# Kernel optimization log

Hardware: AMD Instinct MI355X
Metric: run time of the kernel (lower is better)

## Reference

```python
import jax, jax.numpy as jnp
import numpy as np
import math

B, S, V, E, D, H, L = 1024, 30, 100000, 300, 512, 8, 4
DK = D // H

def setup_inputs() -> dict:
    key = jax.random.key(0)
    ks = jax.random.split(key, 12)
    sc = 0.02
    return {
        "x": jax.random.randint(ks[0], (B, S), 0, V, dtype=jnp.int32),
        "mask": jax.random.randint(ks[1], (B, 1, 1, S), 0, 2, dtype=jnp.int32),
        "emb": jax.random.normal(ks[2], (V, E), dtype=jnp.float32) * sc,
        "W_in": jax.random.normal(ks[3], (D, E), dtype=jnp.float32) * sc,
        "b_in": jnp.zeros((D,), jnp.float32),
        "Wq": jax.random.normal(ks[4], (L, DK, DK), dtype=jnp.float32) * 0.05,
        "Wk": jax.random.normal(ks[5], (L, DK, DK), dtype=jnp.float32) * 0.05,
        "Wv": jax.random.normal(ks[6], (L, DK, DK), dtype=jnp.float32) * 0.05,
        "Wo": jax.random.normal(ks[7], (L, D, D), dtype=jnp.float32) * sc,
        "Wfc": jax.random.normal(ks[8], (L, D, D), dtype=jnp.float32) * sc,
        "bfc": jnp.zeros((L, D), jnp.float32),
        "g1": jnp.ones((L, D), jnp.float32),
        "beta1": jnp.zeros((L, D), jnp.float32),
        "g2": jnp.ones((L, D), jnp.float32),
        "beta2": jnp.zeros((L, D), jnp.float32),
    }

def _layernorm(x, g, b, eps=1e-5):
    mu = jnp.mean(x, axis=-1, keepdims=True)
    var = jnp.mean(jnp.square(x - mu), axis=-1, keepdims=True)
    return (x - mu) * jax.lax.rsqrt(var + eps) * g + b

def _pos_encoding():
    pos = jnp.arange(S, dtype=jnp.float32)[:, None]
    div = jnp.exp(jnp.arange(0, D, 2, dtype=jnp.float32) * (-math.log(10000.0) / D))
    ang = pos * div  # [S, D/2]
    pe = jnp.zeros((S, D), jnp.float32)
    pe = pe.at[:, 0::2].set(jnp.sin(ang)).at[:, 1::2].set(jnp.cos(ang))
    return pe

def _block(h, mask, Wq, Wk, Wv, Wo, Wfc, bfc, g1, b1, g2, b2):
    xh = h.reshape(B, S, H, DK)
    # per-head shared d_k x d_k projections (nn.Linear: y = x @ W.T)
    q = jnp.einsum('bshk,dk->bhsd', xh, Wq)
    k = jnp.einsum('bshk,dk->bhsd', xh, Wk)
    v = jnp.einsum('bshk,dk->bhsd', xh, Wv)
    scores = jnp.einsum('bhqd,bhkd->bhqk', q, k) / math.sqrt(DK)
    scores = jnp.where(mask == 0, jnp.float32(-1e9), scores)
    p = jax.nn.softmax(scores, axis=-1)
    o = jnp.einsum('bhqk,bhkd->bqhd', p, v).reshape(B, S, D)
    o = o @ Wo.T  # output projection, no bias
    n1 = _layernorm(o + h, g1, b1)
    f = n1 @ Wfc.T + bfc
    return _layernorm(f + n1, g2, b2)

def reference(x, mask, emb, W_in, b_in, Wq, Wk, Wv, Wo, Wfc, bfc, g1, beta1, g2, beta2):
    h = emb[x]                               # [B,S,E] embedding gather
    h = jnp.einsum('bse,de->bsd', h, W_in) + b_in
    h = h * math.sqrt(D) + _pos_encoding()[None]  # positional encoding (dropout=eval no-op)
    for i in range(L):
        h = _block(h, mask, Wq[i], Wk[i], Wv[i], Wo[i], Wfc[i], bfc[i],
                   g1[i], beta1[i], g2[i], beta2[i])
    return h
```

## Files before the change

### kernel.cpp

```cpp
#include <hip/hip_runtime.h>
#include <hip/hip_bf16.h>
#include <math.h>

using bf16 = __hip_bfloat16;
typedef __attribute__((ext_vector_type(8))) short short8;
typedef __attribute__((ext_vector_type(4))) float f32x4;

constexpr int nB = 1024, nS = 30, nE = 300, nD = 512, nH = 8, nL = 4, nDK = 64;
constexpr int nTOK = nB * nS;
constexpr float kSqrtD = 22.627416997969522f;
constexpr float kPEc   = -0.03597789207803244f;

__device__ inline unsigned short bfbits(float f) {
  bf16 h = __float2bfloat16(f);
  return *(unsigned short*)&h;
}
__device__ inline void gload16(const void* g, void* lds) {
  __builtin_amdgcn_global_load_lds(
      (const __attribute__((address_space(1))) unsigned int*)g,
      (__attribute__((address_space(3))) unsigned int*)lds, 16, 0, 0);
}

__global__ __launch_bounds__(256) void cvt_kernel(const float* __restrict__ s,
                                                  bf16* __restrict__ d, int n4) {
  int i = blockIdx.x * 256 + threadIdx.x;
  if (i < n4) {
    float4 v = ((const float4*)s)[i];
    ushort4 u;
    u.x = bfbits(v.x); u.y = bfbits(v.y); u.z = bfbits(v.z); u.w = bfbits(v.w);
    ((ushort4*)d)[i] = u;
  }
}

__global__ __launch_bounds__(256) void cvt_pad_win(const float* __restrict__ s,
                                                   bf16* __restrict__ d) {
  int row = blockIdx.x;
  for (int e = threadIdx.x; e < 320; e += 256)
    d[row * 320 + e] = __float2bfloat16((e < nE) ? s[row * nE + e] : 0.f);
}

__global__ __launch_bounds__(256) void pe_kernel(float* __restrict__ pe) {
  int s = blockIdx.x;
  for (int dd = threadIdx.x; dd < nD; dd += 256) {
    float ang = (float)s * expf((float)(dd >> 1) * kPEc);
    pe[s * nD + dd] = (dd & 1) ? cosf(ang) : sinf(ang);
  }
}

__global__ __launch_bounds__(256) void gather_kernel(const int* __restrict__ x,
                                                     const float* __restrict__ emb,
                                                     bf16* __restrict__ a) {
  int g = blockIdx.x * 256 + threadIdx.x;
  int t = g / 40, ch = g - 40 * t;
  float4 v0 = make_float4(0.f, 0.f, 0.f, 0.f), v1 = v0;
  const float* src = emb + (size_t)x[t] * nE + ch * 8;
  if (ch < 37) { v0 = *(const float4*)src; v1 = *(const float4*)(src + 4); }
  else if (ch == 37) { v0 = *(const float4*)src; }
  ushort4 u0, u1;
  u0.x = bfbits(v0.x); u0.y = bfbits(v0.y); u0.z = bfbits(v0.z); u0.w = bfbits(v0.w);
  u1.x = bfbits(v1.x); u1.y = bfbits(v1.y); u1.z = bfbits(v1.z); u1.w = bfbits(v1.w);
  bf16* dst = a + (size_t)t * 320 + ch * 8;
  *(ushort4*)dst = u0;
  *(ushort4*)(dst + 4) = u1;
}

template <int KA, int EPI>
__global__ __launch_bounds__(256, 2) void gemm_fused(
    const bf16* __restrict__ A, const bf16* __restrict__ W,
    const float* __restrict__ bias, const float* __restrict__ resid,
    const float* __restrict__ pe, const float* __restrict__ g,
    const float* __restrict__ beta, float* __restrict__ outf,
    bf16* __restrict__ outb) {
  __shared__ __align__(16) char smem[76288];
  float* tb = (float*)smem;
  float* stats = (float*)(smem + 73728);
  float* stats2 = (float*)(smem + 75776);

  const int tid = threadIdx.x, lane = tid & 63, w = tid >> 6;
  const int q = lane >> 4, c = lane & 15;
  const int m0 = blockIdx.x * 64;
  constexpr int NK = KA / 32;

  f32x4 acc[4][8];
#pragma unroll
  for (int i = 0; i < 4; ++i)
#pragma unroll
    for (int j = 0; j < 8; ++j) acc[i][j] = (f32x4){0.f, 0.f, 0.f, 0.f};

  const bf16* Ag = A + (size_t)(m0 + lane) * KA + w * 8;
  const bf16* Wg = W + (size_t)lane * KA + w * 8;

  auto stage = [&](int ks, int buf) {
    bf16* As = (bf16*)(smem + buf * 36864);
    bf16* Ws = As + 2048;
    gload16(Ag + ks * 32, As + (w * 64) * 8);
#pragma unroll
    for (int j = 0; j < 8; ++j)
      gload16(Wg + (size_t)(j * 64) * KA + ks * 32, Ws + ((size_t)(w * 512 + j * 64)) * 8);
  };

  stage(0, 0);
  for (int ks = 0; ks < NK; ++ks) {
    const int cur = ks & 1;
    if (ks + 1 < NK) {
      stage(ks + 1, cur ^ 1);
      asm volatile("s_waitcnt vmcnt(9)" ::: "memory");
    } else {
      asm volatile("s_waitcnt vmcnt(0)" ::: "memory");
    }
    __builtin_amdgcn_s_barrier();
    asm volatile("" ::: "memory");
    const bf16* As = (const bf16*)(smem + cur * 36864);
    const bf16* Ws = As + 2048;
    short8 af[4], bfr[8];
#pragma unroll
    for (int mt = 0; mt < 4; ++mt)
      af[mt] = *(const short8*)(As + (q * 64 + mt * 16 + c) * 8);
#pragma unroll
    for (int nt = 0; nt < 8; ++nt)
      bfr[nt] = *(const short8*)(Ws + (q * 512 + w * 128 + nt * 16 + c) * 8);
#pragma unroll
    for (int mt = 0; mt < 4; ++mt)
#pragma unroll
      for (int nt = 0; nt < 8; ++nt)
        acc[mt][nt] = __builtin_amdgcn_mfma_f32_16x16x32_bf16(af[mt], bfr[nt], acc[mt][nt], 0, 0, 0);
    asm volatile("" ::: "memory");
    __builtin_amdgcn_s_barrier();
    asm volatile("" ::: "memory");
  }

  float bias4[8];
#pragma unroll
  for (int nt = 0; nt < 8; ++nt)
    bias4[nt] = bias ? bias[w * 128 + nt * 16 + c] : 0.f;

  if (EPI == 0) {
#pragma unroll
    for (int mt = 0; mt < 4; ++mt)
#pragma unroll
      for (int r = 0; r < 4; ++r) {
        int m = m0 + mt * 16 + q * 4 + r;
        int s = m % nS;
        const float* pes = pe + (size_t)s * nD + w * 128 + c;
#pragma unroll
        for (int nt = 0; nt < 8; ++nt)
          acc[mt][nt][r] = (acc[mt][nt][r] + bias4[nt]) * kSqrtD + pes[nt * 16];
      }
    __syncthreads();
  } else {
    float rs[4][4], rq[4][4];
#pragma unroll
    for (int mt = 0; mt < 4; ++mt)
#pragma unroll
      for (int r = 0; r < 4; ++r) {
        int m = m0 + mt * 16 + q * 4 + r;
        const float* rp = resid + (size_t)m * nD + w * 128 + c;
        float s1 = 0.f, s2 = 0.f;
#pragma unroll
        for (int nt = 0; nt < 8; ++nt) {
          float t = acc[mt][nt][r] + bias4[nt] + rp[nt * 16];
          acc[mt][nt][r] = t;
          s1 += t; s2 += t * t;
        }
        rs[mt][r] = s1; rq[mt][r] = s2;
      }
#pragma unroll
    for (int mt = 0; mt < 4; ++mt)
#pragma unroll
      for (int r = 0; r < 4; ++r)
#pragma unroll
        for (int off = 1; off < 16; off <<= 1) {
          rs[mt][r] += __shfl_xor(rs[mt][r], off);
          rq[mt][r] += __shfl_xor(rq[mt][r], off);
        }
#pragma unroll
    for (int mt = 0; mt < 4; ++mt)
#pragma unroll
      for (int r = 0; r < 4; ++r)
        if (c == mt * 4 + r) {
          int row = mt * 16 + q * 4 + r;
          stats[row * 8 + w * 2] = rs[mt][r];
          stats[row * 8 + w * 2 + 1] = rq[mt][r];
        }
    __syncthreads();
    if (tid < 64) {
      float su = 0.f, sq = 0.f;
#pragma unroll
      for (int ww = 0; ww < 4; ++ww) {
        su += stats[tid * 8 + ww * 2];
        sq += stats[tid * 8 + ww * 2 + 1];
      }
      float mu = su * (1.f / nD);
      float var = sq * (1.f / nD) - mu * mu;
      stats2[tid * 2] = mu;
      stats2[tid * 2 + 1] = rsqrtf(var + 1e-5f);
    }
    __syncthreads();
  }

  float* tbw = tb + w * 2048;
  const int l32 = lane & 31, hi = lane >> 5;
  const int colw = w * 128 + l32 * 4;
  float4 g4 = make_float4(0, 0, 0, 0), be4 = g4;
  if (EPI == 1) {
    g4 = *(const float4*)&g[colw];
    be4 = *(const float4*)&beta[colw];
  }
#pragma unroll
  for (int mt = 0; mt < 4; ++mt) {
#pragma unroll
    for (int nt = 0; nt < 8; ++nt)
#pragma unroll
      for (int r = 0; r < 4; ++r)
        tbw[(q * 4 + r) * 128 + nt * 16 + c] = acc[mt][nt][r];
#pragma unroll
    for (int i = 0; i < 8; ++i) {
      float4 v = *(const float4*)&tbw[(i * 64 + lane) * 4];
      int rl = mt * 16 + i * 2 + hi;
      int m = m0 + rl;
      float4 y;
      if (EPI == 1) {
        float mu = stats2[rl * 2], inv = stats2[rl * 2 + 1];
        y.x = (v.x - mu) * inv * g4.x + be4.x;
        y.y = (v.y - mu) * inv * g4.y + be4.y;
        y.z = (v.z - mu) * inv * g4.z + be4.z;
        y.w = (v.w - mu) * inv * g4.w + be4.w;
      } else {
        y = v;
      }
      *(float4*)(outf + (size_t)m * nD + colw) = y;
      ushort4 ub;
      ub.x = bfbits(y.x); ub.y = bfbits(y.y); ub.z = bfbits(y.z); ub.w = bfbits(y.w);
      *(ushort4*)(outb + (size_t)m * nD + colw) = ub;
    }
  }
}

__global__ __launch_bounds__(256) void attn_kernel(
    const bf16* __restrict__ wqb, const bf16* __restrict__ wkb,
    const bf16* __restrict__ wvb, const int* __restrict__ mask,
    bf16* __restrict__ hb) {
  const int tid = threadIdx.x, lane = tid & 63, w = tid >> 6;
  const int q = lane >> 4, c = lane & 15;
  const int b = blockIdx.x >> 3, hd = blockIdx.x & 7;

  __shared__ __align__(16) bf16 xs[8][32][8];
  __shared__ __align__(16) bf16 wq[8][64][8];
  __shared__ __align__(16) bf16 wk[8][64][8];
  __shared__ __align__(16) bf16 wv[8][64][8];
  __shared__ __align__(16) bf16 qb[8][32][8];
  __shared__ __align__(16) bf16 kb[8][32][8];
  __shared__ __align__(16) bf16 vt[4][64][8];
  __shared__ __align__(16) bf16 pb[4][32][8];
  __shared__ float ps[32][33];
  __shared__ int msk[32];

  {
    int row = tid & 31, k8 = tid >> 5;
    uint4 z = make_uint4(0, 0, 0, 0);
    if (row < nS)
      z = *(const uint4*)(hb + (size_t)(b * nS + row) * nD + hd * nDK + k8 * 8);
    *(uint4*)&xs[k8][row][0] = z;
  }
#pragma unroll
  for (int i = 0; i < 2; ++i) {
    int s = tid + i * 256;
    int row = s & 63, k8 = s >> 6;
    *(uint4*)&wq[k8][row][0] = *(const uint4*)(wqb + row * 64 + k8 * 8);
    *(uint4*)&wk[k8][row][0] = *(const uint4*)(wkb + row * 64 + k8 * 8);
    *(uint4*)&wv[k8][row][0] = *(const uint4*)(wvb + row * 64 + k8 * 8);
  }
  if (tid < nS) msk[tid] = mask[b * nS + tid];
  __syncthreads();

  f32x4 aq[2], ak[2], av[2];
#pragma unroll
  for (int mt = 0; mt < 2; ++mt) {
    aq[mt] = (f32x4){0.f, 0.f, 0.f, 0.f};
    ak[mt] = aq[mt]; av[mt] = aq[mt];
  }
#pragma unroll
  for (int kc = 0; kc < 2; ++kc) {
    short8 xa0 = *(const short8*)&xs[kc * 4 + q][c][0];
    short8 xa1 = *(const short8*)&xs[kc * 4 + q][16 + c][0];
    short8 wqf = *(const short8*)&wq[kc * 4 + q][w * 16 + c][0];
    short8 wkf = *(const short8*)&wk[kc * 4 + q][w * 16 + c][0];
    short8 wvf = *(const short8*)&wv[kc * 4 + q][w * 16 + c][0];
    aq[0] = __builtin_amdgcn_mfma_f32_16x16x32_bf16(xa0, wqf, aq[0], 0, 0, 0);
    aq[1] = __builtin_amdgcn_mfma_f32_16x16x32_bf16(xa1, wqf, aq[1], 0, 0, 0);
    ak[0] = __builtin_amdgcn_mfma_f32_16x16x32_bf16(xa0, wkf, ak[0], 0, 0, 0);
    ak[1] = __builtin_amdgcn_mfma_f32_16x16x32_bf16(xa1, wkf, ak[1], 0, 0, 0);
    av[0] = __builtin_amdgcn_mfma_f32_16x16x32_bf16(xa0, wvf, av[0], 0, 0, 0);
    av[1] = __builtin_amdgcn_mfma_f32_16x16x32_bf16(xa1, wvf, av[1], 0, 0, 0);
  }
  const int dk = w * 16 + c;
#pragma unroll
  for (int mt = 0; mt < 2; ++mt)
#pragma unroll
    for (int r = 0; r < 4; ++r) {
      int i = mt * 16 + q * 4 + r;
      qb[dk >> 3][i][dk & 7] = __float2bfloat16(aq[mt][r]);
      kb[dk >> 3][i][dk & 7] = __float2bfloat16(ak[mt][r]);
      vt[i >> 3][dk][i & 7] = __float2bfloat16(av[mt][r]);
    }
  __syncthreads();

  {
    f32x4 sc = (f32x4){0.f, 0.f, 0.f, 0.f};
    const int is0 = (w >> 1) * 16, js0 = (w & 1) * 16;
#pragma unroll
    for (int kc = 0; kc < 2; ++kc) {
      short8 a = *(const short8*)&qb[kc * 4 + q][is0 + c][0];
      short8 bb = *(const short8*)&kb[kc * 4 + q][js0 + c][0];
      sc = __builtin_amdgcn_mfma_f32_16x16x32_bf16(a, bb, sc, 0, 0, 0);
    }
    int j = js0 + c;
    bool live = (j < nS) && (msk[j] != 0);
#pragma unroll
    for (int r = 0; r < 4; ++r) {
      int i = is0 + q * 4 + r;
      ps[i][j] = live ? sc[r] * 0.125f : -1e9f;
    }
  }
  __syncthreads();

  if (tid < nS * 8) {
    int r = tid >> 3, cc = tid & 7;
    float m = -1e30f;
    for (int j = cc; j < nS; j += 8) m = fmaxf(m, ps[r][j]);
#pragma unroll
    for (int o = 1; o < 8; o <<= 1) m = fmaxf(m, __shfl_xor(m, o));
    float sum = 0.f;
    for (int j = cc; j < nS; j += 8) sum += __expf(ps[r][j] - m);
#pragma unroll
    for (int o = 1; o < 8; o <<= 1) sum += __shfl_xor(sum, o);
    float inv = 1.f / sum;
    for (int j = cc; j < nS; j += 8)
      pb[j >> 3][r][j & 7] = __float2bfloat16(__expf(ps[r][j] - m) * inv);
    if (cc >= 6) pb[3][r][cc] = __float2bfloat16(0.f);
  }
  __syncthreads();

  {
    f32x4 o0 = (f32x4){0.f, 0.f, 0.f, 0.f}, o1 = o0;
    short8 pa0 = *(const short8*)&pb[q][c][0];
    short8 pa1 = *(const short8*)&pb[q][16 + c][0];
    short8 vb = *(const short8*)&vt[q][w * 16 + c][0];
    o0 = __builtin_amdgcn_mfma_f32_16x16x32_bf16(pa0, vb, o0, 0, 0, 0);
    o1 = __builtin_amdgcn_mfma_f32_16x16x32_bf16(pa1, vb, o1, 0, 0, 0);
#pragma unroll
    for (int r = 0; r < 4; ++r) {
      int i0 = q * 4 + r;
      hb[(size_t)(b * nS + i0) * nD + hd * nDK + dk] = __float2bfloat16(o0[r]);
      int i1 = 16 + q * 4 + r;
      if (i1 < nS)
        hb[(size_t)(b * nS + i1) * nD + hd * nDK + dk] = __float2bfloat16(o1[r]);
    }
  }
}

extern "C" void kernel_launch(void* const* d_in, const int* in_sizes, int n_in,
                              void* d_out, int out_size, void* d_ws, size_t ws_size,
                              hipStream_t stream) {
  const int*   x    = (const int*)d_in[0];
  const int*   mask = (const int*)d_in[1];
  const float* emb  = (const float*)d_in[2];
  const float* W_in = (const float*)d_in[3];
  const float* b_in = (const float*)d_in[4];
  const float* Wq   = (const float*)d_in[5];
  const float* Wk   = (const float*)d_in[6];
  const float* Wv   = (const float*)d_in[7];
  const float* Wo   = (const float*)d_in[8];
  const float* Wfc  = (const float*)d_in[9];
  const float* bfc  = (const float*)d_in[10];
  const float* g1   = (const float*)d_in[11];
  const float* be1  = (const float*)d_in[12];
  const float* g2   = (const float*)d_in[13];
  const float* be2  = (const float*)d_in[14];
  float* h = (float*)d_out;

  char* ws = (char*)d_ws;
  bf16* wo_b  = (bf16*)ws;
  bf16* wfc_b = (bf16*)(ws + 2097152);
  bf16* wq_b  = (bf16*)(ws + 4194304);
  bf16* wk_b  = (bf16*)(ws + 4227072);
  bf16* wv_b  = (bf16*)(ws + 4259840);
  bf16* win_b = (bf16*)(ws + 4292608);
  float* pe   = (float*)(ws + 4620288);
  bf16* a_emb = (bf16*)(ws + 4681728);
  bf16* hb    = (bf16*)(ws + 24342528);

  cvt_kernel<<<1024, 256, 0, stream>>>(Wo, wo_b, 262144);
  cvt_kernel<<<1024, 256, 0, stream>>>(Wfc, wfc_b, 262144);
  cvt_kernel<<<16, 256, 0, stream>>>(Wq, wq_b, 4096);
  cvt_kernel<<<16, 256, 0, stream>>>(Wk, wk_b, 4096);
  cvt_kernel<<<16, 256, 0, stream>>>(Wv, wv_b, 4096);
  cvt_pad_win<<<512, 256, 0, stream>>>(W_in, win_b);
  pe_kernel<<<30, 256, 0, stream>>>(pe);
  gather_kernel<<<4800, 256, 0, stream>>>(x, emb, a_emb);

  gemm_fused<320, 0><<<480, 256, 0, stream>>>(a_emb, win_b, b_in, nullptr, pe,
                                              nullptr, nullptr, h, hb);
  for (int l = 0; l < nL; ++l) {
    attn_kernel<<<nB * nH, 256, 0, stream>>>(wq_b + l * 4096, wk_b + l * 4096,
                                             wv_b + l * 4096, mask, hb);
    gemm_fused<512, 1><<<480, 256, 0, stream>>>(hb, wo_b + (size_t)l * 262144,
                                                nullptr, h, nullptr, g1 + l * nD,
                                                be1 + l * nD, h, hb);
    gemm_fused<512, 1><<<480, 256, 0, stream>>>(hb, wfc_b + (size_t)l * 262144,
                                                bfc + l * nD, h, nullptr, g2 + l * nD,
                                                be2 + l * nD, h, hb);
  }
  (void)in_sizes; (void)n_in; (void)out_size; (void)ws_size;
}
```

Baseline: 740.2 us.

## Split GEMM into 64x128 tiles, move LayerNorm to separate kernel, bf16 residual

The GEMM now uses 64x128 output tiles on a 2D grid with smaller LDS and four-wave occupancy, so the LayerNorm can no longer be fused across the full row. LayerNorm moves into a standalone row kernel. The residual stream is kept in bf16 ping-pong buffers carved out of the output memory instead of fp32 plus a bf16 copy, which cuts epilogue traffic and raises GEMM parallelism. The cost is extra kernel launches and extra read/write passes for LayerNorm, plus lower precision in the residual path.

```diff
diff --git a/kernel.cpp b/kernel.cpp
--- a/kernel.cpp
+++ b/kernel.cpp
@@ -14,6 +14,9 @@
 __device__ inline unsigned short bfbits(float f) {
   bf16 h = __float2bfloat16(f);
   return *(unsigned short*)&h;
+}
+__device__ inline float b2f(short s) {
+  return __uint_as_float(((unsigned)(unsigned short)s) << 16);
 }
 __device__ inline void gload16(const void* g, void* lds) {
   __builtin_amdgcn_global_load_lds(
@@ -65,38 +68,32 @@
 }
 
 template <int KA, int EPI>
-__global__ __launch_bounds__(256, 2) void gemm_fused(
+__global__ __launch_bounds__(256, 4) void gemm_tile(
     const bf16* __restrict__ A, const bf16* __restrict__ W,
-    const float* __restrict__ bias, const float* __restrict__ resid,
-    const float* __restrict__ pe, const float* __restrict__ g,
-    const float* __restrict__ beta, float* __restrict__ outf,
-    bf16* __restrict__ outb) {
-  __shared__ __align__(16) char smem[76288];
-  float* tb = (float*)smem;
-  float* stats = (float*)(smem + 73728);
-  float* stats2 = (float*)(smem + 75776);
-
+    const float* __restrict__ bias, const bf16* __restrict__ resid,
+    const float* __restrict__ pe, bf16* __restrict__ out) {
+  __shared__ __align__(16) char smem[24576];
   const int tid = threadIdx.x, lane = tid & 63, w = tid >> 6;
   const int q = lane >> 4, c = lane & 15;
-  const int m0 = blockIdx.x * 64;
+  const int m0 = blockIdx.x * 64, n0 = blockIdx.y * 128;
   constexpr int NK = KA / 32;
 
-  f32x4 acc[4][8];
+  f32x4 acc[4][2];
 #pragma unroll
   for (int i = 0; i < 4; ++i)
 #pragma unroll
-    for (int j = 0; j < 8; ++j) acc[i][j] = (f32x4){0.f, 0.f, 0.f, 0.f};
-
-  const bf16* Ag = A + (size_t)(m0 + lane) * KA + w * 8;
-  const bf16* Wg = W + (size_t)lane * KA + w * 8;
+    for (int j = 0; j < 2; ++j) acc[i][j] = (f32x4){0.f, 0.f, 0.f, 0.f};
 
   auto stage = [&](int ks, int buf) {
-    bf16* As = (bf16*)(smem + buf * 36864);
-    bf16* Ws = As + 2048;
-    gload16(Ag + ks * 32, As + (w * 64) * 8);
-#pragma unroll
-    for (int j = 0; j < 8; ++j)
-      gload16(Wg + (size_t)(j * 64) * KA + ks * 32, Ws + ((size_t)(w * 512 + j * 64)) * 8);
+    char* base = smem + buf * 12288;
+    gload16(A + (size_t)(m0 + lane) * KA + ks * 32 + w * 8, base + w * 1024);
+#pragma unroll
+    for (int j = 0; j < 2; ++j) {
+      const int idx = w * 2 + j;
+      const int kc = idx >> 1, hal = idx & 1;
+      gload16(W + (size_t)(n0 + hal * 64 + lane) * KA + ks * 32 + kc * 8,
+              base + 4096 + idx * 1024);
+    }
   };
 
   stage(0, 0);
@@ -104,142 +101,127 @@
     const int cur = ks & 1;
     if (ks + 1 < NK) {
       stage(ks + 1, cur ^ 1);
-      asm volatile("s_waitcnt vmcnt(9)" ::: "memory");
+      asm volatile("s_waitcnt vmcnt(3)" ::: "memory");
     } else {
       asm volatile("s_waitcnt vmcnt(0)" ::: "memory");
     }
     __builtin_amdgcn_s_barrier();
     asm volatile("" ::: "memory");
-    const bf16* As = (const bf16*)(smem + cur * 36864);
-    const bf16* Ws = As + 2048;
-    short8 af[4], bfr[8];
+    const bf16* As = (const bf16*)(smem + cur * 12288);
+    const bf16* Ws = (const bf16*)(smem + cur * 12288 + 4096);
+    short8 af[4], bfr[2];
 #pragma unroll
     for (int mt = 0; mt < 4; ++mt)
       af[mt] = *(const short8*)(As + (q * 64 + mt * 16 + c) * 8);
 #pragma unroll
-    for (int nt = 0; nt < 8; ++nt)
-      bfr[nt] = *(const short8*)(Ws + (q * 512 + w * 128 + nt * 16 + c) * 8);
+    for (int nt = 0; nt < 2; ++nt)
+      bfr[nt] = *(const short8*)(Ws + (q * 128 + w * 32 + nt * 16 + c) * 8);
 #pragma unroll
     for (int mt = 0; mt < 4; ++mt)
 #pragma unroll
-      for (int nt = 0; nt < 8; ++nt)
+      for (int nt = 0; nt < 2; ++nt)
         acc[mt][nt] = __builtin_amdgcn_mfma_f32_16x16x32_bf16(af[mt], bfr[nt], acc[mt][nt], 0, 0, 0);
     asm volatile("" ::: "memory");
     __builtin_amdgcn_s_barrier();
     asm volatile("" ::: "memory");
   }
-
-  float bias4[8];
-#pragma unroll
-  for (int nt = 0; nt < 8; ++nt)
-    bias4[nt] = bias ? bias[w * 128 + nt * 16 + c] : 0.f;
-
-  if (EPI == 0) {
-#pragma unroll
-    for (int mt = 0; mt < 4; ++mt)
+  __syncthreads();
+
+  bf16* tb = (bf16*)smem;
+  float bias2[2];
+#pragma unroll
+  for (int nt = 0; nt < 2; ++nt)
+    bias2[nt] = bias ? bias[n0 + w * 32 + nt * 16 + c] : 0.f;
+#pragma unroll
+  for (int mt = 0; mt < 4; ++mt)
+#pragma unroll
+    for (int nt = 0; nt < 2; ++nt)
 #pragma unroll
       for (int r = 0; r < 4; ++r) {
-        int m = m0 + mt * 16 + q * 4 + r;
-        int s = m % nS;
-        const float* pes = pe + (size_t)s * nD + w * 128 + c;
-#pragma unroll
-        for (int nt = 0; nt < 8; ++nt)
-          acc[mt][nt][r] = (acc[mt][nt][r] + bias4[nt]) * kSqrtD + pes[nt * 16];
+        float t = acc[mt][nt][r] + bias2[nt];
+        if (EPI == 0) t *= kSqrtD;
+        tb[(mt * 16 + q * 4 + r) * 136 + w * 32 + nt * 16 + c] = __float2bfloat16(t);
       }
-    __syncthreads();
+  __syncthreads();
+
+  const int row = tid >> 2, c4 = tid & 3;
+  const int gr = m0 + row;
+#pragma unroll
+  for (int i = 0; i < 4; ++i) {
+    const int cols = c4 * 32 + i * 8;
+    short8 v = *(const short8*)&tb[row * 136 + cols];
+    float e[8];
+#pragma unroll
+    for (int j = 0; j < 8; ++j) e[j] = b2f(v[j]);
+    if (EPI == 0) {
+      const float* pp = pe + (size_t)(gr % nS) * nD + n0 + cols;
+      float4 p0 = *(const float4*)pp, p1 = *(const float4*)(pp + 4);
+      e[0] += p0.x; e[1] += p0.y; e[2] += p0.z; e[3] += p0.w;
+      e[4] += p1.x; e[5] += p1.y; e[6] += p1.z; e[7] += p1.w;
+    } else {
+      short8 rv = *(const short8*)(resid + (size_t)gr * nD + n0 + cols);
+#pragma unroll
+      for (int j = 0; j < 8; ++j) e[j] += b2f(rv[j]);
+    }
+    short8 o;
+#pragma unroll
+    for (int j = 0; j < 8; ++j) o[j] = (short)bfbits(e[j]);
+    *(short8*)(out + (size_t)gr * nD + n0 + cols) = o;
+  }
+}
+
+template <int FINAL>
+__global__ __launch_bounds__(256) void ln_bf(
+    const bf16* __restrict__ X, const float* __restrict__ g,
+    const float* __restrict__ bta, bf16* __restrict__ yb,
+    float* __restrict__ yf) {
+  const int w = threadIdx.x >> 6, lane = threadIdx.x & 63;
+  const int row = blockIdx.x * 4 + w;
+  short8 v = *(const short8*)(X + (size_t)row * nD + lane * 8);
+  float e[8];
+  float s = 0.f, sq = 0.f;
+#pragma unroll
+  for (int j = 0; j < 8; ++j) {
+    e[j] = b2f(v[j]);
+    s += e[j]; sq += e[j] * e[j];
+  }
+#pragma unroll
+  for (int off = 1; off < 64; off <<= 1) {
+    s += __shfl_xor(s, off);
+    sq += __shfl_xor(sq, off);
+  }
+  const float mu = s * (1.f / nD);
+  const float var = sq * (1.f / nD) - mu * mu;
+  const float inv = rsqrtf(var + 1e-5f);
+  const float4 g0 = *(const float4*)(g + lane * 8);
+  const float4 g1 = *(const float4*)(g + lane * 8 + 4);
+  const float4 b0 = *(const float4*)(bta + lane * 8);
+  const float4 b1 = *(const float4*)(bta + lane * 8 + 4);
+  float y[8];
+  y[0] = (e[0] - mu) * inv * g0.x + b0.x;
+  y[1] = (e[1] - mu) * inv * g0.y + b0.y;
+  y[2] = (e[2] - mu) * inv * g0.z + b0.z;
+  y[3] = (e[3] - mu) * inv * g0.w + b0.w;
+  y[4] = (e[4] - mu) * inv * g1.x + b1.x;
+  y[5] = (e[5] - mu) * inv * g1.y + b1.y;
+  y[6] = (e[6] - mu) * inv * g1.z + b1.z;
+  y[7] = (e[7] - mu) * inv * g1.w + b1.w;
+  if (FINAL) {
+    float* p = yf + (size_t)row * nD + lane * 8;
+    *(float4*)p = make_float4(y[0], y[1], y[2], y[3]);
+    *(float4*)(p + 4) = make_float4(y[4], y[5], y[6], y[7]);
   } else {
-    float rs[4][4], rq[4][4];
-#pragma unroll
-    for (int mt = 0; mt < 4; ++mt)
-#pragma unroll
-      for (int r = 0; r < 4; ++r) {
-        int m = m0 + mt * 16 + q * 4 + r;
-        const float* rp = resid + (size_t)m * nD + w * 128 + c;
-        float s1 = 0.f, s2 = 0.f;
-#pragma unroll
-        for (int nt = 0; nt < 8; ++nt) {
-          float t = acc[mt][nt][r] + bias4[nt] + rp[nt * 16];
-          acc[mt][nt][r] = t;
-          s1 += t; s2 += t * t;
-        }
-        rs[mt][r] = s1; rq[mt][r] = s2;
-      }
-#pragma unroll
-    for (int mt = 0; mt < 4; ++mt)
-#pragma unroll
-      for (int r = 0; r < 4; ++r)
-#pragma unroll
-        for (int off = 1; off < 16; off <<= 1) {
-          rs[mt][r] += __shfl_xor(rs[mt][r], off);
-          rq[mt][r] += __shfl_xor(rq[mt][r], off);
-        }
-#pragma unroll
-    for (int mt = 0; mt < 4; ++mt)
-#pragma unroll
-      for (int r = 0; r < 4; ++r)
-        if (c == mt * 4 + r) {
-          int row = mt * 16 + q * 4 + r;
-          stats[row * 8 + w * 2] = rs[mt][r];
-          stats[row * 8 + w * 2 + 1] = rq[mt][r];
-        }
-    __syncthreads();
-    if (tid < 64) {
-      float su = 0.f, sq = 0.f;
-#pragma unroll
-      for (int ww = 0; ww < 4; ++ww) {
-        su += stats[tid * 8 + ww * 2];
-        sq += stats[tid * 8 + ww * 2 + 1];
-      }
-      float mu = su * (1.f / nD);
-      float var = sq * (1.f / nD) - mu * mu;
-      stats2[tid * 2] = mu;
-      stats2[tid * 2 + 1] = rsqrtf(var + 1e-5f);
-    }
-    __syncthreads();
-  }
-
-  float* tbw = tb + w * 2048;
-  const int l32 = lane & 31, hi = lane >> 5;
-  const int colw = w * 128 + l32 * 4;
-  float4 g4 = make_float4(0, 0, 0, 0), be4 = g4;
-  if (EPI == 1) {
-    g4 = *(const float4*)&g[colw];
-    be4 = *(const float4*)&beta[colw];
-  }
-#pragma unroll
-  for (int mt = 0; mt < 4; ++mt) {
-#pragma unroll
-    for (int nt = 0; nt < 8; ++nt)
-#pragma unroll
-      for (int r = 0; r < 4; ++r)
-        tbw[(q * 4 + r) * 128 + nt * 16 + c] = acc[mt][nt][r];
-#pragma unroll
-    for (int i = 0; i < 8; ++i) {
-      float4 v = *(const float4*)&tbw[(i * 64 + lane) * 4];
-      int rl = mt * 16 + i * 2 + hi;
-      int m = m0 + rl;
-      float4 y;
-      if (EPI == 1) {
-        float mu = stats2[rl * 2], inv = stats2[rl * 2 + 1];
-        y.x = (v.x - mu) * inv * g4.x + be4.x;
-        y.y = (v.y - mu) * inv * g4.y + be4.y;
-        y.z = (v.z - mu) * inv * g4.z + be4.z;
-        y.w = (v.w - mu) * inv * g4.w + be4.w;
-      } else {
-        y = v;
-      }
-      *(float4*)(outf + (size_t)m * nD + colw) = y;
-      ushort4 ub;
-      ub.x = bfbits(y.x); ub.y = bfbits(y.y); ub.z = bfbits(y.z); ub.w = bfbits(y.w);
-      *(ushort4*)(outb + (size_t)m * nD + colw) = ub;
-    }
+    short8 o;
+#pragma unroll
+    for (int j = 0; j < 8; ++j) o[j] = (short)bfbits(y[j]);
+    *(short8*)(yb + (size_t)row * nD + lane * 8) = o;
   }
 }
 
 __global__ __launch_bounds__(256) void attn_kernel(
     const bf16* __restrict__ wqb, const bf16* __restrict__ wkb,
     const bf16* __restrict__ wvb, const int* __restrict__ mask,
-    bf16* __restrict__ hb) {
+    const bf16* __restrict__ hin, bf16* __restrict__ aout) {
   const int tid = threadIdx.x, lane = tid & 63, w = tid >> 6;
   const int q = lane >> 4, c = lane & 15;
   const int b = blockIdx.x >> 3, hd = blockIdx.x & 7;
@@ -259,7 +241,7 @@
     int row = tid & 31, k8 = tid >> 5;
     uint4 z = make_uint4(0, 0, 0, 0);
     if (row < nS)
-      z = *(const uint4*)(hb + (size_t)(b * nS + row) * nD + hd * nDK + k8 * 8);
+      z = *(const uint4*)(hin + (size_t)(b * nS + row) * nD + hd * nDK + k8 * 8);
     *(uint4*)&xs[k8][row][0] = z;
   }
 #pragma unroll
@@ -351,10 +333,10 @@
 #pragma unroll
     for (int r = 0; r < 4; ++r) {
       int i0 = q * 4 + r;
-      hb[(size_t)(b * nS + i0) * nD + hd * nDK + dk] = __float2bfloat16(o0[r]);
+      aout[(size_t)(b * nS + i0) * nD + hd * nDK + dk] = __float2bfloat16(o0[r]);
       int i1 = 16 + q * 4 + r;
       if (i1 < nS)
-        hb[(size_t)(b * nS + i1) * nD + hd * nDK + dk] = __float2bfloat16(o1[r]);
+        aout[(size_t)(b * nS + i1) * nD + hd * nDK + dk] = __float2bfloat16(o1[r]);
     }
   }
 }
@@ -377,7 +359,9 @@
   const float* be1  = (const float*)d_in[12];
   const float* g2   = (const float*)d_in[13];
   const float* be2  = (const float*)d_in[14];
-  float* h = (float*)d_out;
+
+  bf16* bufA = (bf16*)d_out;
+  bf16* bufB = bufA + (size_t)nTOK * nD;
 
   char* ws = (char*)d_ws;
   bf16* wo_b  = (bf16*)ws;
@@ -388,7 +372,7 @@
   bf16* win_b = (bf16*)(ws + 4292608);
   float* pe   = (float*)(ws + 4620288);
   bf16* a_emb = (bf16*)(ws + 4681728);
-  bf16* hb    = (bf16*)(ws + 24342528);
+  bf16* tmpf  = (bf16*)(ws + 4681728);
 
   cvt_kernel<<<1024, 256, 0, stream>>>(Wo, wo_b, 262144);
   cvt_kernel<<<1024, 256, 0, stream>>>(Wfc, wfc_b, 262144);
@@ -399,17 +383,27 @@
   pe_kernel<<<30, 256, 0, stream>>>(pe);
   gather_kernel<<<4800, 256, 0, stream>>>(x, emb, a_emb);
 
-  gemm_fused<320, 0><<<480, 256, 0, stream>>>(a_emb, win_b, b_in, nullptr, pe,
-                                              nullptr, nullptr, h, hb);
+  const dim3 ggrid(nTOK / 64, nD / 128);
+  gemm_tile<320, 0><<<ggrid, 256, 0, stream>>>(a_emb, win_b, b_in, nullptr, pe, bufA);
+
+  bf16* cur = bufA;
+  bf16* oth = bufB;
   for (int l = 0; l < nL; ++l) {
     attn_kernel<<<nB * nH, 256, 0, stream>>>(wq_b + l * 4096, wk_b + l * 4096,
-                                             wv_b + l * 4096, mask, hb);
-    gemm_fused<512, 1><<<480, 256, 0, stream>>>(hb, wo_b + (size_t)l * 262144,
-                                                nullptr, h, nullptr, g1 + l * nD,
-                                                be1 + l * nD, h, hb);
-    gemm_fused<512, 1><<<480, 256, 0, stream>>>(hb, wfc_b + (size_t)l * 262144,
-                                                bfc + l * nD, h, nullptr, g2 + l * nD,
-                                                be2 + l * nD, h, hb);
+                                             wv_b + l * 4096, mask, cur, oth);
+    gemm_tile<512, 1><<<ggrid, 256, 0, stream>>>(oth, wo_b + (size_t)l * 262144,
+                                                 nullptr, cur, nullptr, cur);
+    ln_bf<0><<<nTOK / 4, 256, 0, stream>>>(cur, g1 + l * nD, be1 + l * nD, cur, nullptr);
+    bf16* o2 = (l == nL - 1) ? tmpf : oth;
+    gemm_tile<512, 1><<<ggrid, 256, 0, stream>>>(cur, wfc_b + (size_t)l * 262144,
+                                                 bfc + l * nD, cur, nullptr, o2);
+    if (l < nL - 1) {
+      ln_bf<0><<<nTOK / 4, 256, 0, stream>>>(oth, g2 + l * nD, be2 + l * nD, oth, nullptr);
+      bf16* t = cur; cur = oth; oth = t;
+    } else {
+      ln_bf<1><<<nTOK / 4, 256, 0, stream>>>(tmpf, g2 + l * nD, be2 + l * nD,
+                                             nullptr, (float*)d_out);
+    }
   }
   (void)in_sizes; (void)n_in; (void)out_size; (void)ws_size;
 }
```

Measured after the change: 812.5 us. 9.8% more time.
